# Performance work log

Measured on AMD Instinct MI355X. Metric: run time of the kernel, lower is better.

## Reference

```python
import jax, jax.numpy as jnp
import numpy as np

S, B, D, E, H, REQ = 2048, 4, 256, 256, 8, 16  # seq, batch, hidden_dim, embed(=hidden_size), heads, band half-width


def setup_inputs() -> dict:
    key = jax.random.key(0)
    ks = jax.random.split(key, 12)
    w = lambda k, shape: jax.random.normal(k, shape, jnp.float32) * 0.02
    return {
        "mod": jax.random.normal(ks[0], (S, B, D), jnp.float32),
        "mask": jnp.zeros((B, S), jnp.float32),  # unused in speaker=False branch (kept for fidelity)
        "Wq": w(ks[1], (E, D)), "bq": jnp.zeros((E,), jnp.float32),
        "Wk": w(ks[2], (E, D)), "bk": jnp.zeros((E,), jnp.float32),
        "Wv": w(ks[3], (E, D)), "bv": jnp.zeros((E,), jnp.float32),
        "Win": w(ks[4], (3 * E, E)), "bin_": jnp.zeros((3 * E,), jnp.float32),  # MHA in_proj
        "Wout": w(ks[5], (E, E)), "bout": jnp.zeros((E,), jnp.float32),         # MHA out_proj
        "Wfc": w(ks[6], (D, E)), "bfc": jnp.zeros((D,), jnp.float32),           # self.fc
        "gamma": jnp.ones((D,), jnp.float32), "beta": jnp.zeros((D,), jnp.float32),
        "req": REQ,
    }


def reference(mod, mask, Wq, bq, Wk, bk, Wv, bv, Win, bin_, Wout, bout, Wfc, bfc, gamma, beta, req):
    s, b, d = mod.shape
    e = Wq.shape[0]
    hd = e // H
    # fc_q/k/v (pre-projection) then MultiheadAttention's own in_proj
    q = mod @ Wq.T + bq                       # (s, b, e)
    k = mod @ Wk.T + bk
    v = mod @ Wv.T + bv
    q = q @ Win[:e].T + bin_[:e]
    k = k @ Win[e:2 * e].T + bin_[e:2 * e]
    v = v @ Win[2 * e:].T + bin_[2 * e:]
    split = lambda x: x.reshape(s, b, H, hd).transpose(1, 2, 0, 3)  # (b, H, s, hd)
    qh, kh, vh = split(q), split(k), split(v)
    scores = jnp.einsum('bhqd,bhkd->bhqk', qh, kh) / jnp.sqrt(jnp.float32(hd))
    idx = jnp.arange(s)
    allowed = jnp.abs(idx[:, None] - idx[None, :]) < req  # band: diag + offsets 1..req-1
    scores = jnp.where(allowed[None, None], scores, -jnp.inf)
    attn = jax.nn.softmax(scores, axis=-1)                # attn dropout = identity (eval)
    ctx = jnp.einsum('bhqk,bhkd->bhqd', attn, vh)
    ctx = ctx.transpose(2, 0, 1, 3).reshape(s, b, e)
    ctx = ctx @ Wout.T + bout
    y = ctx @ Wfc.T + bfc + mod                           # dropout(0.5) = identity (eval), residual
    mu = jnp.mean(y, axis=-1, keepdims=True)
    var = jnp.var(y, axis=-1, keepdims=True)
    return (y - mu) / jnp.sqrt(var + 1e-6) * gamma + beta
```

## Files before the change

kernel.cpp:

```cpp
#include <hip/hip_runtime.h>
#include <hip/hip_bf16.h>
#include <math.h>

#define SS 2048
#define BB 4
#define DD 256
#define EE 256
#define HH 8
#define HD 32
#define TT (SS*BB)

typedef unsigned short ushortt;
typedef __attribute__((ext_vector_type(8))) short short8;
typedef __attribute__((ext_vector_type(4))) float f32x4;

__device__ __forceinline__ float bfbits2f(ushortt u) {
    return __uint_as_float(((unsigned int)u) << 16);
}
__device__ __forceinline__ ushortt f2bf_bits(float f) {
    unsigned int u = __float_as_uint(f);
    unsigned int r = u + 0x7FFFu + ((u >> 16) & 1u);
    return (ushortt)(r >> 16);
}

__device__ __forceinline__ int robust_req(const void* p) {
    int i = *(const int*)p;
    if (i >= 1 && i <= SS) return i;
    float f = __int_as_float(i);
    if (f >= 1.f && f <= (float)SS) return (int)(f + 0.5f);
    float b = bfbits2f(*(const ushortt*)p);
    if (b >= 1.f && b <= (float)SS) return (int)(b + 0.5f);
    return 16;
}

__global__ __launch_bounds__(256)
void fuse_conv(const float* __restrict__ mod,
               const float* __restrict__ Win,
               const float* __restrict__ Wq, const float* __restrict__ Wk,
               const float* __restrict__ Wv,
               const float* __restrict__ bq, const float* __restrict__ bk,
               const float* __restrict__ bv, const float* __restrict__ bin_,
               const float* __restrict__ Wfc, const float* __restrict__ Wout,
               const float* __restrict__ bout, const float* __restrict__ bfc,
               ushortt* __restrict__ Weffb, float* __restrict__ beff,
               ushortt* __restrict__ W2b, float* __restrict__ b2,
               ushortt* __restrict__ modb) {
    __shared__ float red[4];
    const int t = threadIdx.x;

    {
        size_t base = (size_t)blockIdx.x * 2048 + (size_t)t * 8;
        float4 v0 = *(const float4*)(mod + base);
        float4 v1 = *(const float4*)(mod + base + 4);
        ushort4 o0, o1;
        o0.x = f2bf_bits(v0.x); o0.y = f2bf_bits(v0.y);
        o0.z = f2bf_bits(v0.z); o0.w = f2bf_bits(v0.w);
        o1.x = f2bf_bits(v1.x); o1.y = f2bf_bits(v1.y);
        o1.z = f2bf_bits(v1.z); o1.w = f2bf_bits(v1.w);
        *(ushort4*)(modb + base)     = o0;
        *(ushort4*)(modb + base + 4) = o1;
    }

    float tb;
    if (blockIdx.x < 3 * EE) {
        int r = blockIdx.x;
        int i = r / EE;
        const float* Wi = (i == 0) ? Wq : ((i == 1) ? Wk : Wv);
        const float* bi = (i == 0) ? bq : ((i == 1) ? bk : bv);
        float acc = 0.f;
        for (int e1 = 0; e1 < EE; ++e1) acc += Win[r * EE + e1] * Wi[e1 * DD + t];
        Weffb[(size_t)r * DD + t] = f2bf_bits(acc);
        tb = Win[r * EE + t] * bi[t];
    } else {
        int d = blockIdx.x - 3 * EE;
        float acc = 0.f;
        for (int e = 0; e < EE; ++e) acc += Wfc[d * EE + e] * Wout[e * EE + t];
        W2b[(size_t)d * EE + t] = f2bf_bits(acc);
        tb = Wfc[d * EE + t] * bout[t];
    }
#pragma unroll
    for (int off = 32; off >= 1; off >>= 1) tb += __shfl_xor(tb, off);
    if ((t & 63) == 0) red[t >> 6] = tb;
    __syncthreads();
    if (t == 0) {
        float s = red[0] + red[1] + red[2] + red[3];
        if (blockIdx.x < 3 * EE) beff[blockIdx.x] = s + bin_[blockIdx.x];
        else                     b2[blockIdx.x - 3 * EE] = s + bfc[blockIdx.x - 3 * EE];
    }
}

__global__ __launch_bounds__(256)
void gemm_qkv(const ushortt* __restrict__ A, const ushortt* __restrict__ Bw,
              const float* __restrict__ bias, ushortt* __restrict__ C) {
    __shared__ __align__(16) ushortt Blds[96][264];
    const int t    = threadIdx.x;
    const int lane = t & 63;
    const int w    = t >> 6;
    const int quad = lane >> 4;
    const int l16  = lane & 15;
    const int n0   = blockIdx.x * 96;
    const int m0   = blockIdx.y * 64;
    const int N    = 3 * EE, K = DD;

    short8 af[8];
    const ushortt* arow = A + (size_t)(m0 + w * 16 + l16) * K + quad * 8;
#pragma unroll
    for (int kf = 0; kf < 8; ++kf)
        af[kf] = *(const short8*)(arow + kf * 32);

#pragma unroll
    for (int i = 0; i < 12; ++i) {
        int slot = t + 256 * i;
        int row  = slot >> 5;
        int c8   = (slot & 31) * 8;
        *(float4*)&Blds[row][c8] = *(const float4*)(Bw + (size_t)(n0 + row) * K + c8);
    }
    __syncthreads();

    f32x4 acc[6];
#pragma unroll
    for (int fn = 0; fn < 6; ++fn) acc[fn] = (f32x4){0.f, 0.f, 0.f, 0.f};

#pragma unroll
    for (int fn = 0; fn < 6; ++fn)
#pragma unroll
        for (int kf = 0; kf < 8; ++kf) {
            short8 bfr = *(const short8*)&Blds[fn * 16 + l16][kf * 32 + quad * 8];
            acc[fn] = __builtin_amdgcn_mfma_f32_16x16x32_bf16(af[kf], bfr, acc[fn], 0, 0, 0);
        }

#pragma unroll
    for (int fn = 0; fn < 6; ++fn)
#pragma unroll
        for (int r = 0; r < 4; ++r) {
            int row = m0 + w * 16 + quad * 4 + r;
            int col = n0 + fn * 16 + l16;
            C[(size_t)row * N + col] = f2bf_bits(acc[fn][r] + bias[col]);
        }
}

__global__ __launch_bounds__(256)
void attn_mfma(const ushortt* __restrict__ qkv,
               const void* __restrict__ reqp,
               ushortt* __restrict__ ctx) {
    __shared__ __align__(16) ushortt Plds[4][16 * 72];
    const int t    = threadIdx.x;
    const int w    = t >> 6;
    const int lane = t & 63;
    const int l16  = lane & 15;
    const int quad = lane >> 4;
    const int wid  = blockIdx.x * 4 + w;
    const int stile = wid >> 5;
    const int rem   = wid & 31;
    const int b = rem >> 3;
    const int h = rem & 7;
    const int s0 = stile * 16;
    const int req = robust_req(reqp);

    const ushortt* qptr = qkv + ((size_t)(s0 + l16) * BB + b) * (3 * EE) + h * HD + quad * 8;
    short8 aq = *(const short8*)qptr;

    f32x4 sc[3];
#pragma unroll
    for (int kt = 0; kt < 3; ++kt) {
        int j = s0 - 16 + kt * 16 + l16;
        int jc = min(max(j, 0), SS - 1);
        const ushortt* kp = qkv + ((size_t)jc * BB + b) * (3 * EE) + EE + h * HD + quad * 8;
        short8 bk = *(const short8*)kp;
        sc[kt] = __builtin_amdgcn_mfma_f32_16x16x32_bf16(aq, bk, (f32x4){0.f,0.f,0.f,0.f}, 0, 0, 0);
    }

    const float scale = 0.17677669529663687f;
    float pv[3][4];
#pragma unroll
    for (int r = 0; r < 4; ++r) {
        int s = s0 + quad * 4 + r;
        float vv[3];
        float mx = -INFINITY;
#pragma unroll
        for (int kt = 0; kt < 3; ++kt) {
            int j = s0 - 16 + kt * 16 + l16;
            int dj = s - j;
            bool valid = (j >= 0) && (j < SS) && (dj < req) && (-dj < req);
            vv[kt] = valid ? sc[kt][r] * scale : -INFINITY;
            mx = fmaxf(mx, vv[kt]);
        }
#pragma unroll
        for (int off = 1; off <= 8; off <<= 1) mx = fmaxf(mx, __shfl_xor(mx, off));
        float sum = 0.f;
#pragma unroll
        for (int kt = 0; kt < 3; ++kt) {
            float p = (vv[kt] > -INFINITY) ? __expf(vv[kt] - mx) : 0.f;
            pv[kt][r] = p;
            sum += p;
        }
#pragma unroll
        for (int off = 1; off <= 8; off <<= 1) sum += __shfl_xor(sum, off);
        float inv = 1.f / sum;
#pragma unroll
        for (int kt = 0; kt < 3; ++kt) pv[kt][r] *= inv;
    }

    ushortt* P = &Plds[w][0];
#pragma unroll
    for (int kt = 0; kt < 3; ++kt)
#pragma unroll
        for (int r = 0; r < 4; ++r)
            P[(quad * 4 + r) * 72 + kt * 16 + l16] = f2bf_bits(pv[kt][r]);
#pragma unroll
    for (int r = 0; r < 4; ++r)
        P[(quad * 4 + r) * 72 + 48 + l16] = 0;
    __syncthreads();

    short8 pa[2];
    pa[0] = *(const short8*)&P[l16 * 72 + quad * 8];
    pa[1] = *(const short8*)&P[l16 * 72 + 32 + quad * 8];

    f32x4 acc[2];
    acc[0] = (f32x4){0.f,0.f,0.f,0.f};
    acc[1] = (f32x4){0.f,0.f,0.f,0.f};
#pragma unroll
    for (int c = 0; c < 2; ++c) {
#pragma unroll
        for (int nd = 0; nd < 2; ++nd) {
            short8 bv;
#pragma unroll
            for (int u = 0; u < 8; ++u) {
                int j = s0 - 16 + c * 32 + quad * 8 + u;
                int jc = min(max(j, 0), SS - 1);
                bv[u] = (short)qkv[((size_t)jc * BB + b) * (3 * EE) + 2 * EE + h * HD + nd * 16 + l16];
            }
            acc[nd] = __builtin_amdgcn_mfma_f32_16x16x32_bf16(pa[c], bv, acc[nd], 0, 0, 0);
        }
    }

#pragma unroll
    for (int nd = 0; nd < 2; ++nd)
#pragma unroll
        for (int r = 0; r < 4; ++r) {
            int tok = (s0 + quad * 4 + r) * BB + b;
            ctx[(size_t)tok * EE + h * HD + nd * 16 + l16] = f2bf_bits(acc[nd][r]);
        }
}

__global__ __launch_bounds__(256)
void gemm_tail_ln(const ushortt* __restrict__ A, const ushortt* __restrict__ Bw,
                  const float* __restrict__ b2, const float* __restrict__ mod,
                  const float* __restrict__ gamma, const float* __restrict__ beta,
                  float* __restrict__ out) {
    __shared__ __align__(16) ushortt Alds[32][72];
    __shared__ __align__(16) ushortt Blds[256][72];
    __shared__ float part1[4][32], part2[4][32];
    const int t    = threadIdx.x;
    const int lane = t & 63;
    const int w    = t >> 6;
    const int quad = lane >> 4;
    const int l16  = lane & 15;
    const int m0   = blockIdx.x * 32;
    const int K    = EE;

    f32x4 acc[2][4];
#pragma unroll
    for (int fm = 0; fm < 2; ++fm)
#pragma unroll
        for (int fn = 0; fn < 4; ++fn) acc[fm][fn] = (f32x4){0.f,0.f,0.f,0.f};

    for (int k0 = 0; k0 < K; k0 += 64) {
        {
            int row = t >> 3, c8 = (t & 7) * 8;
            *(float4*)&Alds[row][c8] = *(const float4*)(A + (size_t)(m0 + row) * K + k0 + c8);
        }
#pragma unroll
        for (int i = 0; i < 8; ++i) {
            int slot = t + 256 * i;
            int row = slot >> 3, c8 = (slot & 7) * 8;
            *(float4*)&Blds[row][c8] = *(const float4*)(Bw + (size_t)row * K + k0 + c8);
        }
        __syncthreads();
        short8 af[2][2], bfr[4][2];
#pragma unroll
        for (int fm = 0; fm < 2; ++fm)
#pragma unroll
            for (int kf = 0; kf < 2; ++kf)
                af[fm][kf] = *(const short8*)&Alds[fm * 16 + l16][kf * 32 + quad * 8];
#pragma unroll
        for (int fn = 0; fn < 4; ++fn)
#pragma unroll
            for (int kf = 0; kf < 2; ++kf)
                bfr[fn][kf] = *(const short8*)&Blds[w * 64 + fn * 16 + l16][kf * 32 + quad * 8];
#pragma unroll
        for (int kf = 0; kf < 2; ++kf)
#pragma unroll
            for (int fm = 0; fm < 2; ++fm)
#pragma unroll
                for (int fn = 0; fn < 4; ++fn)
                    acc[fm][fn] = __builtin_amdgcn_mfma_f32_16x16x32_bf16(
                        af[fm][kf], bfr[fn][kf], acc[fm][fn], 0, 0, 0);
        __syncthreads();
    }

#pragma unroll
    for (int fm = 0; fm < 2; ++fm) {
#pragma unroll
        for (int r = 0; r < 4; ++r) {
            int rowl = fm * 16 + quad * 4 + r;
            int row  = m0 + rowl;
            float s1 = 0.f, s2 = 0.f;
#pragma unroll
            for (int fn = 0; fn < 4; ++fn) {
                int col = w * 64 + fn * 16 + l16;
                float v = acc[fm][fn][r] + b2[col] + mod[(size_t)row * DD + col];
                acc[fm][fn][r] = v;
                s1 += v;
                s2 += v * v;
            }
#pragma unroll
            for (int off = 1; off <= 8; off <<= 1) {
                s1 += __shfl_xor(s1, off);
                s2 += __shfl_xor(s2, off);
            }
            if (l16 == 0) { part1[w][rowl] = s1; part2[w][rowl] = s2; }
        }
    }
    __syncthreads();
#pragma unroll
    for (int fm = 0; fm < 2; ++fm) {
#pragma unroll
        for (int r = 0; r < 4; ++r) {
            int rowl = fm * 16 + quad * 4 + r;
            int row  = m0 + rowl;
            float S1 = part1[0][rowl] + part1[1][rowl] + part1[2][rowl] + part1[3][rowl];
            float S2 = part2[0][rowl] + part2[1][rowl] + part2[2][rowl] + part2[3][rowl];
            float mean = S1 * (1.f / DD);
            float var  = S2 * (1.f / DD) - mean * mean;
            float inv  = rsqrtf(var + 1e-6f);
#pragma unroll
            for (int fn = 0; fn < 4; ++fn) {
                int col = w * 64 + fn * 16 + l16;
                out[(size_t)row * DD + col] = (acc[fm][fn][r] - mean) * inv * gamma[col] + beta[col];
            }
        }
    }
}

extern "C" void kernel_launch(void* const* d_in, const int* in_sizes, int n_in,
                              void* d_out, int out_size, void* d_ws, size_t ws_size,
                              hipStream_t stream) {
    const float* mod  = (const float*)d_in[0];
    const float* Wq   = (const float*)d_in[2];
    const float* bq   = (const float*)d_in[3];
    const float* Wk   = (const float*)d_in[4];
    const float* bk   = (const float*)d_in[5];
    const float* Wv   = (const float*)d_in[6];
    const float* bv   = (const float*)d_in[7];
    const float* Win  = (const float*)d_in[8];
    const float* bin_ = (const float*)d_in[9];
    const float* Wout = (const float*)d_in[10];
    const float* bout = (const float*)d_in[11];
    const float* Wfc  = (const float*)d_in[12];
    const float* bfc  = (const float*)d_in[13];
    const float* gamma= (const float*)d_in[14];
    const float* beta = (const float*)d_in[15];
    const void*  reqp = d_in[16];

    float* out = (float*)d_out;

    float*  beff = (float*)d_ws;
    float*  b2   = beff + 3 * EE;
    ushortt* Weffb = (ushortt*)(b2 + DD);
    ushortt* W2b   = Weffb + 3 * EE * DD;
    ushortt* modb  = W2b + DD * EE;
    ushortt* qkvb  = modb + (size_t)TT * DD;
    ushortt* ctxb  = qkvb + (size_t)TT * 3 * EE;

    fuse_conv<<<1024, 256, 0, stream>>>(mod, Win, Wq, Wk, Wv, bq, bk, bv, bin_,
                                        Wfc, Wout, bout, bfc,
                                        Weffb, beff, W2b, b2, modb);
    gemm_qkv<<<dim3(8, TT / 64), 256, 0, stream>>>(modb, Weffb, beff, qkvb);
    attn_mfma<<<4096 / 4, 256, 0, stream>>>(qkvb, reqp, ctxb);
    gemm_tail_ln<<<TT / 32, 256, 0, stream>>>(ctxb, W2b, b2, mod, gamma, beta, out);
}
```

Before: 134.1 us.

## Fold weight products with tiled MFMA and read QKV B fragments directly from global

The weight-folding kernel previously used 1024 blocks, each computing one output row with a scalar fp32 dot-product loop. It now uses 64 blocks that each convert a 64x64 tile of both operands to bf16 in shared memory and run MFMA; the other blocks return right after the mod->bf16 cast. The QKV GEMM drops its shared-memory B staging and barrier, and each wave loads B fragments straight from global memory, relying on cache reuse. The fold now rounds its inputs to bf16, which costs some precision, and the direct global loads may raise memory traffic.

```diff
diff --git a/kernel.cpp b/kernel.cpp
--- a/kernel.cpp
+++ b/kernel.cpp
@@ -34,7 +34,7 @@
 }
 
 __global__ __launch_bounds__(256)
-void fuse_conv(const float* __restrict__ mod,
+void fuse_fold(const float* __restrict__ mod,
                const float* __restrict__ Win,
                const float* __restrict__ Wq, const float* __restrict__ Wk,
                const float* __restrict__ Wv,
@@ -45,7 +45,8 @@
                ushortt* __restrict__ Weffb, float* __restrict__ beff,
                ushortt* __restrict__ W2b, float* __restrict__ b2,
                ushortt* __restrict__ modb) {
-    __shared__ float red[4];
+    __shared__ __align__(16) ushortt ALds[64][264];
+    __shared__ __align__(16) ushortt BLds[64][264];
     const int t = threadIdx.x;
 
     {
@@ -60,80 +61,123 @@
         *(ushort4*)(modb + base)     = o0;
         *(ushort4*)(modb + base + 4) = o1;
     }
-
-    float tb;
-    if (blockIdx.x < 3 * EE) {
-        int r = blockIdx.x;
-        int i = r / EE;
-        const float* Wi = (i == 0) ? Wq : ((i == 1) ? Wk : Wv);
-        const float* bi = (i == 0) ? bq : ((i == 1) ? bk : bv);
-        float acc = 0.f;
-        for (int e1 = 0; e1 < EE; ++e1) acc += Win[r * EE + e1] * Wi[e1 * DD + t];
-        Weffb[(size_t)r * DD + t] = f2bf_bits(acc);
-        tb = Win[r * EE + t] * bi[t];
-    } else {
-        int d = blockIdx.x - 3 * EE;
-        float acc = 0.f;
-        for (int e = 0; e < EE; ++e) acc += Wfc[d * EE + e] * Wout[e * EE + t];
-        W2b[(size_t)d * EE + t] = f2bf_bits(acc);
-        tb = Wfc[d * EE + t] * bout[t];
-    }
-#pragma unroll
-    for (int off = 32; off >= 1; off >>= 1) tb += __shfl_xor(tb, off);
-    if ((t & 63) == 0) red[t >> 6] = tb;
+    if (blockIdx.x >= 64) return;
+
+    const int mat = blockIdx.x >> 4;
+    const int mt  = (blockIdx.x >> 2) & 3;
+    const int nt  = blockIdx.x & 3;
+    const int m0  = mt * 64, n0 = nt * 64;
+
+    const float* Asrc = (mat == 3) ? (Wfc + (size_t)m0 * EE)
+                                   : (Win + ((size_t)mat * EE + m0) * EE);
+    const float* Bsrc = (mat == 0) ? Wq : (mat == 1) ? Wk : (mat == 2) ? Wv : Wout;
+
+#pragma unroll
+    for (int i = 0; i < 16; ++i) {
+        int slot = t + 256 * i;
+        int row = slot >> 6, c4 = slot & 63;
+        float4 v = *(const float4*)(Asrc + (size_t)row * EE + c4 * 4);
+        ushort4 o;
+        o.x = f2bf_bits(v.x); o.y = f2bf_bits(v.y);
+        o.z = f2bf_bits(v.z); o.w = f2bf_bits(v.w);
+        *(ushort4*)&ALds[row][c4 * 4] = o;
+    }
+#pragma unroll
+    for (int i = 0; i < 16; ++i) {
+        int slot = t + 256 * i;
+        int k = slot >> 4, c4 = slot & 15;
+        float4 v = *(const float4*)(Bsrc + (size_t)k * DD + n0 + c4 * 4);
+        BLds[c4 * 4 + 0][k] = f2bf_bits(v.x);
+        BLds[c4 * 4 + 1][k] = f2bf_bits(v.y);
+        BLds[c4 * 4 + 2][k] = f2bf_bits(v.z);
+        BLds[c4 * 4 + 3][k] = f2bf_bits(v.w);
+    }
+    if (nt == 0) {
+        const float* bvec = (mat == 0) ? bq : (mat == 1) ? bk : (mat == 2) ? bv : bout;
+        int r = t >> 2, qq = t & 3;
+        const float* arow = Asrc + (size_t)r * EE + qq * 64;
+        const float* bv64 = bvec + qq * 64;
+        float p = 0.f;
+#pragma unroll
+        for (int j = 0; j < 64; ++j) p += arow[j] * bv64[j];
+        p += __shfl_xor(p, 1);
+        p += __shfl_xor(p, 2);
+        if (qq == 0) {
+            if (mat == 3) b2[m0 + r] = p + bfc[m0 + r];
+            else          beff[mat * EE + m0 + r] = p + bin_[mat * EE + m0 + r];
+        }
+    }
     __syncthreads();
-    if (t == 0) {
-        float s = red[0] + red[1] + red[2] + red[3];
-        if (blockIdx.x < 3 * EE) beff[blockIdx.x] = s + bin_[blockIdx.x];
-        else                     b2[blockIdx.x - 3 * EE] = s + bfc[blockIdx.x - 3 * EE];
-    }
+
+    const int w = t >> 6, lane = t & 63, quad = lane >> 4, l16 = lane & 15;
+    const int wm = w >> 1, wn = w & 1;
+    f32x4 acc[2][2];
+#pragma unroll
+    for (int fm = 0; fm < 2; ++fm)
+#pragma unroll
+        for (int fn = 0; fn < 2; ++fn) acc[fm][fn] = (f32x4){0.f, 0.f, 0.f, 0.f};
+#pragma unroll
+    for (int kf = 0; kf < 8; ++kf) {
+        short8 af0 = *(const short8*)&ALds[wm * 32 + l16][kf * 32 + quad * 8];
+        short8 af1 = *(const short8*)&ALds[wm * 32 + 16 + l16][kf * 32 + quad * 8];
+        short8 bf0 = *(const short8*)&BLds[wn * 32 + l16][kf * 32 + quad * 8];
+        short8 bf1 = *(const short8*)&BLds[wn * 32 + 16 + l16][kf * 32 + quad * 8];
+        acc[0][0] = __builtin_amdgcn_mfma_f32_16x16x32_bf16(af0, bf0, acc[0][0], 0, 0, 0);
+        acc[0][1] = __builtin_amdgcn_mfma_f32_16x16x32_bf16(af0, bf1, acc[0][1], 0, 0, 0);
+        acc[1][0] = __builtin_amdgcn_mfma_f32_16x16x32_bf16(af1, bf0, acc[1][0], 0, 0, 0);
+        acc[1][1] = __builtin_amdgcn_mfma_f32_16x16x32_bf16(af1, bf1, acc[1][1], 0, 0, 0);
+    }
+    ushortt* Cd = (mat == 3) ? W2b : (Weffb + (size_t)mat * EE * DD);
+#pragma unroll
+    for (int fm = 0; fm < 2; ++fm)
+#pragma unroll
+        for (int fn = 0; fn < 2; ++fn)
+#pragma unroll
+            for (int r = 0; r < 4; ++r) {
+                int row = m0 + wm * 32 + fm * 16 + quad * 4 + r;
+                int col = n0 + wn * 32 + fn * 16 + l16;
+                Cd[(size_t)row * DD + col] = f2bf_bits(acc[fm][fn][r]);
+            }
 }
 
 __global__ __launch_bounds__(256)
 void gemm_qkv(const ushortt* __restrict__ A, const ushortt* __restrict__ Bw,
               const float* __restrict__ bias, ushortt* __restrict__ C) {
-    __shared__ __align__(16) ushortt Blds[96][264];
     const int t    = threadIdx.x;
     const int lane = t & 63;
     const int w    = t >> 6;
     const int quad = lane >> 4;
     const int l16  = lane & 15;
     const int n0   = blockIdx.x * 96;
-    const int m0   = blockIdx.y * 64;
+    const int m0   = blockIdx.y * 64 + w * 16;
     const int N    = 3 * EE, K = DD;
 
     short8 af[8];
-    const ushortt* arow = A + (size_t)(m0 + w * 16 + l16) * K + quad * 8;
+    const ushortt* arow = A + (size_t)(m0 + l16) * K + quad * 8;
 #pragma unroll
     for (int kf = 0; kf < 8; ++kf)
         af[kf] = *(const short8*)(arow + kf * 32);
 
-#pragma unroll
-    for (int i = 0; i < 12; ++i) {
-        int slot = t + 256 * i;
-        int row  = slot >> 5;
-        int c8   = (slot & 31) * 8;
-        *(float4*)&Blds[row][c8] = *(const float4*)(Bw + (size_t)(n0 + row) * K + c8);
-    }
-    __syncthreads();
-
     f32x4 acc[6];
 #pragma unroll
     for (int fn = 0; fn < 6; ++fn) acc[fn] = (f32x4){0.f, 0.f, 0.f, 0.f};
 
 #pragma unroll
+    for (int fn = 0; fn < 6; ++fn) {
+        const ushortt* brow = Bw + (size_t)(n0 + fn * 16 + l16) * K + quad * 8;
+#pragma unroll
+        for (int kf = 0; kf < 8; ++kf) {
+            short8 bfr = *(const short8*)(brow + kf * 32);
+            acc[fn] = __builtin_amdgcn_mfma_f32_16x16x32_bf16(af[kf], bfr, acc[fn], 0, 0, 0);
+        }
+    }
+
+#pragma unroll
     for (int fn = 0; fn < 6; ++fn)
 #pragma unroll
-        for (int kf = 0; kf < 8; ++kf) {
-            short8 bfr = *(const short8*)&Blds[fn * 16 + l16][kf * 32 + quad * 8];
-            acc[fn] = __builtin_amdgcn_mfma_f32_16x16x32_bf16(af[kf], bfr, acc[fn], 0, 0, 0);
-        }
-
-#pragma unroll
-    for (int fn = 0; fn < 6; ++fn)
-#pragma unroll
         for (int r = 0; r < 4; ++r) {
-            int row = m0 + w * 16 + quad * 4 + r;
+            int row = (m0 & ~15) + quad * 4 + r + (m0 & 15);
+            row = m0 + quad * 4 + r;
             int col = n0 + fn * 16 + l16;
             C[(size_t)row * N + col] = f2bf_bits(acc[fn][r] + bias[col]);
         }
@@ -373,7 +417,7 @@
     ushortt* qkvb  = modb + (size_t)TT * DD;
     ushortt* ctxb  = qkvb + (size_t)TT * 3 * EE;
 
-    fuse_conv<<<1024, 256, 0, stream>>>(mod, Win, Wq, Wk, Wv, bq, bk, bv, bin_,
+    fuse_fold<<<1024, 256, 0, stream>>>(mod, Win, Wq, Wk, Wv, bq, bk, bv, bin_,
                                         Wfc, Wout, bout, bfc,
                                         Weffb, beff, W2b, b2, modb);
     gemm_qkv<<<dim3(8, TT / 64), 256, 0, stream>>>(modb, Weffb, beff, qkvb);
```

After: 146.1 us. +8.9%, slower.
